# Kernel tuning notes

Hardware: AMD Instinct MI355X
Metric: run time of the kernel (lower is better)

## Reference

```python
import jax, jax.numpy as jnp
import numpy as np

EMBED_DIM = 1024
NUM_HEADS = 16
HEAD_DIM = EMBED_DIM // NUM_HEADS


def setup_inputs() -> dict:
    key = jax.random.key(0)
    ks = jax.random.split(key, 9)
    B, S, E = 4, 2048, EMBED_DIM
    scale = 1.0 / np.sqrt(E)
    x = jax.random.normal(ks[0], (B, S, E), dtype=jnp.float32)
    # Linear layers: weight [E, E] (out, in) and bias [E], torch-style init scale
    Wq = jax.random.uniform(ks[1], (E, E), jnp.float32, -scale, scale)
    bq = jax.random.uniform(ks[2], (E,), jnp.float32, -scale, scale)
    Wk = jax.random.uniform(ks[3], (E, E), jnp.float32, -scale, scale)
    bk = jax.random.uniform(ks[4], (E,), jnp.float32, -scale, scale)
    Wv = jax.random.uniform(ks[5], (E, E), jnp.float32, -scale, scale)
    bv = jax.random.uniform(ks[6], (E,), jnp.float32, -scale, scale)
    Wo = jax.random.uniform(ks[7], (E, E), jnp.float32, -scale, scale)
    bo = jax.random.uniform(ks[8], (E,), jnp.float32, -scale, scale)
    return {"x": x, "Wq": Wq, "bq": bq, "Wk": Wk, "bk": bk,
            "Wv": Wv, "bv": bv, "Wo": Wo, "bo": bo}


def reference(x, Wq, bq, Wk, bk, Wv, bv, Wo, bo):
    B, S, E = x.shape
    H, D = NUM_HEADS, HEAD_DIM

    def proj(W, b):
        # torch Linear: x @ W.T + b ; reshape to [B, H, S, D]
        y = jnp.einsum('bse,fe->bsf', x, W) + b
        return y.reshape(B, S, H, D).transpose(0, 2, 1, 3)

    Q = proj(Wq, bq)
    K = proj(Wk, bk)
    V = proj(Wv, bv)
    scores = jnp.einsum('bhqd,bhkd->bhqk', Q, K) / jnp.sqrt(
        jnp.asarray(D, dtype=jnp.float32))
    attn = jax.nn.softmax(scores, axis=-1)
    out = jnp.einsum('bhqk,bhkd->bhqd', attn, V)
    out = out.transpose(0, 2, 1, 3).reshape(B, S, E)
    out = jnp.einsum('bse,fe->bsf', out, Wo) + bo
    return out
```

## Files before the change

kernel.cpp:

```cpp
#include <hip/hip_runtime.h>
#include <math.h>

#define SEQ 2048
#define EMB 1024
#define NH 16
#define HD 64
#define BATCH 4
#define MROWS (BATCH * SEQ)

typedef unsigned short u16;
typedef unsigned int u32;
typedef _Float16 f16;
using half8   = __attribute__((ext_vector_type(8))) f16;
using fp16x2  = __attribute__((ext_vector_type(2))) __fp16;
using vfloat4 = __attribute__((ext_vector_type(4))) float;

__device__ __forceinline__ u16 f2h(float f) {
    union { f16 h; u16 u; } x; x.h = (f16)f; return x.u;
}
__device__ __forceinline__ u32 pk2h(float a, float b) {
    union { fp16x2 h; u32 u; } x;
    x.h = __builtin_amdgcn_cvt_pkrtz(a, b);
    return x.u;
}
__device__ __forceinline__ float exp2v(float x) {
    float r; asm("v_exp_f32 %0, %1" : "=v"(r) : "v"(x)); return r;
}

__device__ __forceinline__ void gload16(const void* g, void* l) {
    __builtin_amdgcn_global_load_lds(
        (const __attribute__((address_space(1))) void*)g,
        (__attribute__((address_space(3))) void*)l, 16, 0, 0);
}

__global__ __launch_bounds__(256) void cvt5_kernel(
    const float* __restrict__ x,  const float* __restrict__ wq,
    const float* __restrict__ wk, const float* __restrict__ wv,
    const float* __restrict__ wo,
    uint2* __restrict__ xh, uint2* __restrict__ wqkv, uint2* __restrict__ woh)
{
    int gid = blockIdx.x * 256 + threadIdx.x;
    const float4* src; uint2* dst; int o;
    if (gid < (1 << 21)) {
        src = (const float4*)x; dst = xh; o = gid;
    } else {
        int g = gid - (1 << 21);
        int r = g >> 18;
        o = g & ((1 << 18) - 1);
        if      (r == 0) { src = (const float4*)wq; dst = wqkv; }
        else if (r == 1) { src = (const float4*)wk; dst = wqkv + (1 << 18); }
        else if (r == 2) { src = (const float4*)wv; dst = wqkv + (2 << 18); }
        else             { src = (const float4*)wo; dst = woh; }
    }
    float4 v = src[o];
    dst[o] = make_uint2(pk2h(v.x, v.y), pk2h(v.z, v.w));
}

__global__ __launch_bounds__(256) void gemm_qkv_kernel(
    const u16* __restrict__ A, const u16* __restrict__ Wqkv,
    const float* __restrict__ bq, const float* __restrict__ bk,
    const float* __restrict__ bv,
    u16* __restrict__ Qo, u16* __restrict__ Ko, u16* __restrict__ Vo,
    float sq)
{
    __shared__ char lds[32768];
    const int tid = threadIdx.x, wave = tid >> 6, lane = tid & 63;
    const int bm = blockIdx.y, bn = blockIdx.x;
    const int mat = bn >> 3;
    const int wr = wave >> 1, wc = wave & 1;

    const int srow  = wave * 16 + (lane >> 2);
    const int sslot = lane & 3;
    const int ldso  = wave * 1024 + (lane << 4);
    const u16* Ab = A    + (size_t)bm * 128 * EMB;
    const u16* Wb = Wqkv + (size_t)bn * 128 * EMB;

    vfloat4 acc[4][4] = {};

#define QKV_STAGE(k0, bufi)                                                   \
    {                                                                         \
        char* Ad = lds + (bufi) * 16384;                                      \
        char* Bd = Ad + 8192;                                                 \
        _Pragma("unroll")                                                     \
        for (int i2 = 0; i2 < 2; ++i2) {                                      \
            int row = i2 * 64 + srow;                                         \
            int ko  = ((sslot ^ ((row >> 1) & 3)) << 3);                      \
            gload16(Ab + (size_t)row * EMB + (k0) + ko, Ad + i2 * 4096 + ldso); \
            gload16(Wb + (size_t)row * EMB + (k0) + ko, Bd + i2 * 4096 + ldso); \
        }                                                                     \
    }

    QKV_STAGE(0, 0);
    __syncthreads();

    for (int it = 0; it < EMB / 32; ++it) {
        const int cur = it & 1;
        if (it + 1 < EMB / 32) QKV_STAGE((it + 1) * 32, cur ^ 1);

        char* As = lds + cur * 16384;
        char* Bs = As + 8192;
        half8 af[4], bfr[4];
        #pragma unroll
        for (int m = 0; m < 4; ++m) {
            int r = wr * 64 + m * 16 + (lane & 15);
            af[m] = *(const half8*)(As + r * 64 + ((((lane >> 4) ^ ((r >> 1) & 3)) << 4)));
        }
        #pragma unroll
        for (int n = 0; n < 4; ++n) {
            int r = wc * 64 + n * 16 + (lane & 15);
            bfr[n] = *(const half8*)(Bs + r * 64 + ((((lane >> 4) ^ ((r >> 1) & 3)) << 4)));
        }
        #pragma unroll
        for (int m = 0; m < 4; ++m)
            #pragma unroll
            for (int n = 0; n < 4; ++n)
                acc[m][n] = __builtin_amdgcn_mfma_f32_16x16x32_f16(af[m], bfr[n], acc[m][n], 0, 0, 0);

        __syncthreads();
    }
#undef QKV_STAGE

    const float* bp = (mat == 0) ? bq : ((mat == 1) ? bk : bv);
    const float scale = (mat == 0) ? sq : 1.0f;
    u16* Co = (mat == 0) ? Qo : ((mat == 1) ? Ko : Vo);
    const int row0 = bm * 128 + wr * 64;
    const int col0 = (bn & 7) * 128 + wc * 64;

    #pragma unroll
    for (int n = 0; n < 4; ++n) {
        int col = col0 + n * 16 + (lane & 15);
        float bb = bp[col];
        int h = col >> 6, d = col & 63;
        if (mat != 2) {
            #pragma unroll
            for (int m = 0; m < 4; ++m)
                #pragma unroll
                for (int j = 0; j < 4; ++j) {
                    int row = row0 + m * 16 + (lane >> 4) * 4 + j;
                    int b = row >> 11, s = row & (SEQ - 1);
                    Co[(((size_t)(b * NH + h)) * SEQ + s) * HD + d] =
                        f2h((acc[m][n][j] + bb) * scale);
                }
        } else {
            #pragma unroll
            for (int m = 0; m < 4; ++m) {
                int row = row0 + m * 16 + (lane >> 4) * 4;
                int b = row >> 11, s = row & (SEQ - 1);
                u32 w0 = pk2h(acc[m][n][0] + bb, acc[m][n][1] + bb);
                u32 w1 = pk2h(acc[m][n][2] + bb, acc[m][n][3] + bb);
                *(uint2*)(Co + (((size_t)(b * NH + h)) * HD + d) * SEQ + s) =
                    make_uint2(w0, w1);
            }
        }
    }
}

__global__ __launch_bounds__(256) void gemm_f16_kernel(
    const u16* __restrict__ A, const u16* __restrict__ W,
    const float* __restrict__ bias, float* __restrict__ C)
{
    __shared__ char lds[32768];
    const int tid = threadIdx.x, wave = tid >> 6, lane = tid & 63;
    const int bm = blockIdx.y, bn = blockIdx.x;
    const int wr = wave >> 1, wc = wave & 1;

    const int srow  = wave * 16 + (lane >> 2);
    const int sslot = lane & 3;
    const int ldso  = wave * 1024 + (lane << 4);
    const u16* Ab = A + (size_t)bm * 128 * EMB;
    const u16* Wb = W + (size_t)bn * 128 * EMB;

    vfloat4 acc[4][4] = {};

#define F16_STAGE(k0, bufi)                                                   \
    {                                                                         \
        char* Ad = lds + (bufi) * 16384;                                      \
        char* Bd = Ad + 8192;                                                 \
        _Pragma("unroll")                                                     \
        for (int i2 = 0; i2 < 2; ++i2) {                                      \
            int row = i2 * 64 + srow;                                         \
            int ko  = ((sslot ^ ((row >> 1) & 3)) << 3);                      \
            gload16(Ab + (size_t)row * EMB + (k0) + ko, Ad + i2 * 4096 + ldso); \
            gload16(Wb + (size_t)row * EMB + (k0) + ko, Bd + i2 * 4096 + ldso); \
        }                                                                     \
    }

    F16_STAGE(0, 0);
    __syncthreads();

    for (int it = 0; it < EMB / 32; ++it) {
        const int cur = it & 1;
        if (it + 1 < EMB / 32) F16_STAGE((it + 1) * 32, cur ^ 1);

        char* As = lds + cur * 16384;
        char* Bs = As + 8192;
        half8 af[4], bfr[4];
        #pragma unroll
        for (int m = 0; m < 4; ++m) {
            int r = wr * 64 + m * 16 + (lane & 15);
            af[m] = *(const half8*)(As + r * 64 + ((((lane >> 4) ^ ((r >> 1) & 3)) << 4)));
        }
        #pragma unroll
        for (int n = 0; n < 4; ++n) {
            int r = wc * 64 + n * 16 + (lane & 15);
            bfr[n] = *(const half8*)(Bs + r * 64 + ((((lane >> 4) ^ ((r >> 1) & 3)) << 4)));
        }
        #pragma unroll
        for (int m = 0; m < 4; ++m)
            #pragma unroll
            for (int n = 0; n < 4; ++n)
                acc[m][n] = __builtin_amdgcn_mfma_f32_16x16x32_f16(af[m], bfr[n], acc[m][n], 0, 0, 0);

        __syncthreads();
    }
#undef F16_STAGE

    const int row0 = bm * 128 + wr * 64, col0 = bn * 128 + wc * 64;
    #pragma unroll
    for (int n = 0; n < 4; ++n) {
        int col = col0 + n * 16 + (lane & 15);
        float bb = bias[col];
        #pragma unroll
        for (int m = 0; m < 4; ++m)
            #pragma unroll
            for (int j = 0; j < 4; ++j) {
                int row = row0 + m * 16 + (lane >> 4) * 4 + j;
                C[(size_t)row * EMB + col] = acc[m][n][j] + bb;
            }
    }
}

__device__ __forceinline__ void stage_rows(const u16* g, int rstride, char* dst,
                                           int wave, int lane) {
    int r = wave * 8 + (lane >> 3), sl = lane & 7;
    #pragma unroll
    for (int i2 = 0; i2 < 2; ++i2) {
        int row = i2 * 32 + r;
        gload16(g + (size_t)row * rstride + ((sl ^ (row & 7)) << 3),
                dst + i2 * 4096 + wave * 1024 + (lane << 4));
    }
}

__global__ __launch_bounds__(256) void attn_kernel(
    const u16* __restrict__ Q, const u16* __restrict__ K,
    const u16* __restrict__ Vt, u16* __restrict__ O)
{
    __shared__ char lds[40960];
    char* QPs = lds;
    char* Kb0 = lds + 8192;
    char* Kb1 = lds + 16384;
    char* Vb0 = lds + 24576;
    char* Vb1 = lds + 32768;

    const int tid = threadIdx.x, wave = tid >> 6, lane = tid & 63;
    const int c = lane >> 4, li = lane & 15;

    const int swz = (blockIdx.x & 7) * 128 + (blockIdx.x >> 3);
    const int bh = swz >> 4;
    const int q0 = (swz & 15) << 7;

    const u16* Qg = Q  + ((size_t)bh * SEQ + q0) * HD;
    const u16* Kg = K  + (size_t)bh * SEQ * HD;
    const u16* Vg = Vt + (size_t)bh * HD * SEQ;

    stage_rows(Qg, HD, QPs, wave, lane);
    stage_rows(Kg, HD, Kb0, wave, lane);
    stage_rows(Vg, SEQ, Vb0, wave, lane);
    __syncthreads();

    half8 qf[2][2];
    const int q = wave * 16 + li;
    #pragma unroll
    for (int cc = 0; cc < 2; ++cc)
        qf[0][cc] = *(const half8*)(QPs + q * 128 + (((4 * cc + c) ^ (q & 7)) << 4));
    __syncthreads();
    stage_rows(Qg + (size_t)64 * HD, HD, QPs, wave, lane);
    __syncthreads();
    #pragma unroll
    for (int cc = 0; cc < 2; ++cc)
        qf[1][cc] = *(const half8*)(QPs + q * 128 + (((4 * cc + c) ^ (q & 7)) << 4));

    const half8 ones8 = {1, 1, 1, 1, 1, 1, 1, 1};
    char* Pw = QPs + wave * 2048;
    vfloat4 o0[4] = {}, o1[4] = {};
    vfloat4 l0 = {}, l1 = {};

    for (int kt = 0; kt < SEQ / 64; ++kt) {
        char* Kc = (kt & 1) ? Kb1 : Kb0;
        char* Vc = (kt & 1) ? Vb1 : Vb0;
        if (kt < SEQ / 64 - 1) {
            stage_rows(Kg + (size_t)(kt + 1) * 64 * HD, HD,
                       (kt & 1) ? Kb0 : Kb1, wave, lane);
            stage_rows(Vg + (kt + 1) * 64, SEQ,
                       (kt & 1) ? Vb0 : Vb1, wave, lane);
        }

        vfloat4 s0[4] = {}, s1[4] = {};
        __builtin_amdgcn_s_setprio(1);
        #pragma unroll
        for (int n = 0; n < 4; ++n) {
            int key = 16 * n + li;
            #pragma unroll
            for (int cc = 0; cc < 2; ++cc) {
                half8 kb = *(const half8*)(Kc + key * 128 + (((4 * cc + c) ^ (li & 7)) << 4));
                s0[n] = __builtin_amdgcn_mfma_f32_16x16x32_f16(kb, qf[0][cc], s0[n], 0, 0, 0);
                s1[n] = __builtin_amdgcn_mfma_f32_16x16x32_f16(kb, qf[1][cc], s1[n], 0, 0, 0);
            }
        }
        __builtin_amdgcn_s_setprio(0);

        #pragma unroll
        for (int n = 0; n < 4; ++n)
            #pragma unroll
            for (int j = 0; j < 4; ++j) {
                s0[n][j] = exp2v(s0[n][j]);
                s1[n][j] = exp2v(s1[n][j]);
            }

        half8 pf0[2], pf1[2];
        #pragma unroll
        for (int n = 0; n < 4; ++n) {
            u32 w0 = pk2h(s0[n][0], s0[n][1]);
            u32 w1 = pk2h(s0[n][2], s0[n][3]);
            *(uint2*)(Pw + li * 128 + (((2 * n + (c >> 1)) ^ (li & 7)) << 4) + ((c & 1) << 3))
                = make_uint2(w0, w1);
        }
        #pragma unroll
        for (int cc = 0; cc < 2; ++cc)
            pf0[cc] = *(const half8*)(Pw + li * 128 + (((4 * cc + c) ^ (li & 7)) << 4));
        #pragma unroll
        for (int n = 0; n < 4; ++n) {
            u32 w0 = pk2h(s1[n][0], s1[n][1]);
            u32 w1 = pk2h(s1[n][2], s1[n][3]);
            *(uint2*)(Pw + li * 128 + (((2 * n + (c >> 1)) ^ (li & 7)) << 4) + ((c & 1) << 3))
                = make_uint2(w0, w1);
        }
        #pragma unroll
        for (int cc = 0; cc < 2; ++cc)
            pf1[cc] = *(const half8*)(Pw + li * 128 + (((4 * cc + c) ^ (li & 7)) << 4));

        __builtin_amdgcn_s_setprio(1);
        #pragma unroll
        for (int n = 0; n < 4; ++n) {
            int r = 16 * n + li;
            #pragma unroll
            for (int cc = 0; cc < 2; ++cc) {
                half8 vf = *(const half8*)(Vc + r * 128 + (((4 * cc + c) ^ (li & 7)) << 4));
                o0[n] = __builtin_amdgcn_mfma_f32_16x16x32_f16(vf, pf0[cc], o0[n], 0, 0, 0);
                o1[n] = __builtin_amdgcn_mfma_f32_16x16x32_f16(vf, pf1[cc], o1[n], 0, 0, 0);
            }
        }
        #pragma unroll
        for (int cc = 0; cc < 2; ++cc) {
            l0 = __builtin_amdgcn_mfma_f32_16x16x32_f16(ones8, pf0[cc], l0, 0, 0, 0);
            l1 = __builtin_amdgcn_mfma_f32_16x16x32_f16(ones8, pf1[cc], l1, 0, 0, 0);
        }
        __builtin_amdgcn_s_setprio(0);

        __syncthreads();
    }

    const int b = bh >> 4, h = bh & 15;
    const size_t r0 = ((size_t)b * SEQ + q0 + wave * 16 + li) * EMB + h * 64;
    const size_t r1 = ((size_t)b * SEQ + q0 + 64 + wave * 16 + li) * EMB + h * 64;
    float i0 = 1.0f / l0[0];
    float i1 = 1.0f / l1[0];
    #pragma unroll
    for (int n = 0; n < 4; ++n) {
        *(uint2*)(O + r0 + 16 * n + 4 * c) =
            make_uint2(pk2h(o0[n][0] * i0, o0[n][1] * i0),
                       pk2h(o0[n][2] * i0, o0[n][3] * i0));
        *(uint2*)(O + r1 + 16 * n + 4 * c) =
            make_uint2(pk2h(o1[n][0] * i1, o1[n][1] * i1),
                       pk2h(o1[n][2] * i1, o1[n][3] * i1));
    }
}

extern "C" void kernel_launch(void* const* d_in, const int* in_sizes, int n_in,
                              void* d_out, int out_size, void* d_ws, size_t ws_size,
                              hipStream_t stream) {
    const float* x  = (const float*)d_in[0];
    const float* Wq = (const float*)d_in[1];
    const float* bq = (const float*)d_in[2];
    const float* Wk = (const float*)d_in[3];
    const float* bk = (const float*)d_in[4];
    const float* Wv = (const float*)d_in[5];
    const float* bv = (const float*)d_in[6];
    const float* Wo = (const float*)d_in[7];
    const float* bo = (const float*)d_in[8];
    float* out = (float*)d_out;

    char* ws = (char*)d_ws;
    u16* xh   = (u16*)(ws);
    u16* Qh   = (u16*)(ws + ((size_t)16 << 20));
    u16* Kh   = (u16*)(ws + ((size_t)32 << 20));
    u16* Vh   = (u16*)(ws + ((size_t)48 << 20));
    u16* Ah   = (u16*)(ws + ((size_t)64 << 20));
    u16* Wqkv = (u16*)(ws + ((size_t)80 << 20));
    u16* Woh  = (u16*)(ws + ((size_t)88 << 20));

    const int nCvt = (1 << 21) + (1 << 20);

    cvt5_kernel<<<nCvt / 256, 256, 0, stream>>>(
        x, Wq, Wk, Wv, Wo, (uint2*)xh, (uint2*)Wqkv, (uint2*)Woh);

    const float SCALE_Q = 0.125f * 1.4426950408889634f;
    gemm_qkv_kernel<<<dim3(3 * EMB / 128, MROWS / 128), 256, 0, stream>>>(
        xh, Wqkv, bq, bk, bv, Qh, Kh, Vh, SCALE_Q);

    attn_kernel<<<dim3(SEQ / 128 * BATCH * NH), 256, 0, stream>>>(Qh, Kh, Vh, Ah);

    gemm_f16_kernel<<<dim3(EMB / 128, MROWS / 128), 256, 0, stream>>>(Ah, Woh, bo, out);
}
```

Measured before the change: 214.6 us.

## Split P scratch into two buffers and use partial vmcnt waits with raw barriers

Gives each of the two query halves its own LDS region for the P tile, so both writes can be issued before both reads instead of a serialised write-read-write-read on one buffer. The full __syncthreads at the end of each key tile is replaced by raw s_barrier instructions plus an explicit s_waitcnt vmcnt(4) at the top of the loop. This lets the prefetch of the next K/V tile stay in flight while the current tile is consumed. It raises LDS use from 40 KB to 48 KB, which may lower occupancy, and correctness depends on the hand-counted vmcnt matching the number of outstanding global-to-LDS loads.

New measurement: 219.9 us. 2.5% more time.

```diff
diff --git a/kernel.cpp b/kernel.cpp
--- a/kernel.cpp
+++ b/kernel.cpp
@@ -245,12 +245,13 @@
     const u16* __restrict__ Q, const u16* __restrict__ K,
     const u16* __restrict__ Vt, u16* __restrict__ O)
 {
-    __shared__ char lds[40960];
-    char* QPs = lds;
-    char* Kb0 = lds + 8192;
-    char* Kb1 = lds + 16384;
-    char* Vb0 = lds + 24576;
-    char* Vb1 = lds + 32768;
+    __shared__ char lds[49152];
+    char* Ps0 = lds;
+    char* Ps1 = lds + 8192;
+    char* Kb0 = lds + 16384;
+    char* Kb1 = lds + 24576;
+    char* Vb0 = lds + 32768;
+    char* Vb1 = lds + 40960;
 
     const int tid = threadIdx.x, wave = tid >> 6, lane = tid & 63;
     const int c = lane >> 4, li = lane & 15;
@@ -263,7 +264,7 @@
     const u16* Kg = K  + (size_t)bh * SEQ * HD;
     const u16* Vg = Vt + (size_t)bh * HD * SEQ;
 
-    stage_rows(Qg, HD, QPs, wave, lane);
+    stage_rows(Qg, HD, Ps0, wave, lane);
     stage_rows(Kg, HD, Kb0, wave, lane);
     stage_rows(Vg, SEQ, Vb0, wave, lane);
     __syncthreads();
@@ -272,16 +273,17 @@
     const int q = wave * 16 + li;
     #pragma unroll
     for (int cc = 0; cc < 2; ++cc)
-        qf[0][cc] = *(const half8*)(QPs + q * 128 + (((4 * cc + c) ^ (q & 7)) << 4));
+        qf[0][cc] = *(const half8*)(Ps0 + q * 128 + (((4 * cc + c) ^ (q & 7)) << 4));
     __syncthreads();
-    stage_rows(Qg + (size_t)64 * HD, HD, QPs, wave, lane);
+    stage_rows(Qg + (size_t)64 * HD, HD, Ps0, wave, lane);
     __syncthreads();
     #pragma unroll
     for (int cc = 0; cc < 2; ++cc)
-        qf[1][cc] = *(const half8*)(QPs + q * 128 + (((4 * cc + c) ^ (q & 7)) << 4));
+        qf[1][cc] = *(const half8*)(Ps0 + q * 128 + (((4 * cc + c) ^ (q & 7)) << 4));
 
     const half8 ones8 = {1, 1, 1, 1, 1, 1, 1, 1};
-    char* Pw = QPs + wave * 2048;
+    char* Pw0 = Ps0 + wave * 2048;
+    char* Pw1 = Ps1 + wave * 2048;
     vfloat4 o0[4] = {}, o1[4] = {};
     vfloat4 l0 = {}, l1 = {};
 
@@ -293,7 +295,12 @@
                        (kt & 1) ? Kb0 : Kb1, wave, lane);
             stage_rows(Vg + (kt + 1) * 64, SEQ,
                        (kt & 1) ? Vb0 : Vb1, wave, lane);
-        }
+            asm volatile("s_waitcnt vmcnt(4)" ::: "memory");
+        } else {
+            asm volatile("s_waitcnt vmcnt(0)" ::: "memory");
+        }
+        __builtin_amdgcn_sched_barrier(0);
+        asm volatile("s_barrier" ::: "memory");
 
         vfloat4 s0[4] = {}, s1[4] = {};
         __builtin_amdgcn_s_setprio(1);
@@ -317,27 +324,19 @@
                 s1[n][j] = exp2v(s1[n][j]);
             }
 
+        #pragma unroll
+        for (int n = 0; n < 4; ++n) {
+            *(uint2*)(Pw0 + li * 128 + (((2 * n + (c >> 1)) ^ (li & 7)) << 4) + ((c & 1) << 3))
+                = make_uint2(pk2h(s0[n][0], s0[n][1]), pk2h(s0[n][2], s0[n][3]));
+            *(uint2*)(Pw1 + li * 128 + (((2 * n + (c >> 1)) ^ (li & 7)) << 4) + ((c & 1) << 3))
+                = make_uint2(pk2h(s1[n][0], s1[n][1]), pk2h(s1[n][2], s1[n][3]));
+        }
         half8 pf0[2], pf1[2];
         #pragma unroll
-        for (int n = 0; n < 4; ++n) {
-            u32 w0 = pk2h(s0[n][0], s0[n][1]);
-            u32 w1 = pk2h(s0[n][2], s0[n][3]);
-            *(uint2*)(Pw + li * 128 + (((2 * n + (c >> 1)) ^ (li & 7)) << 4) + ((c & 1) << 3))
-                = make_uint2(w0, w1);
-        }
-        #pragma unroll
-        for (int cc = 0; cc < 2; ++cc)
-            pf0[cc] = *(const half8*)(Pw + li * 128 + (((4 * cc + c) ^ (li & 7)) << 4));
-        #pragma unroll
-        for (int n = 0; n < 4; ++n) {
-            u32 w0 = pk2h(s1[n][0], s1[n][1]);
-            u32 w1 = pk2h(s1[n][2], s1[n][3]);
-            *(uint2*)(Pw + li * 128 + (((2 * n + (c >> 1)) ^ (li & 7)) << 4) + ((c & 1) << 3))
-                = make_uint2(w0, w1);
-        }
-        #pragma unroll
-        for (int cc = 0; cc < 2; ++cc)
-            pf1[cc] = *(const half8*)(Pw + li * 128 + (((4 * cc + c) ^ (li & 7)) << 4));
+        for (int cc = 0; cc < 2; ++cc) {
+            pf0[cc] = *(const half8*)(Pw0 + li * 128 + (((4 * cc + c) ^ (li & 7)) << 4));
+            pf1[cc] = *(const half8*)(Pw1 + li * 128 + (((4 * cc + c) ^ (li & 7)) << 4));
+        }
 
         __builtin_amdgcn_s_setprio(1);
         #pragma unroll
@@ -357,7 +356,7 @@
         }
         __builtin_amdgcn_s_setprio(0);
 
-        __syncthreads();
+        asm volatile("s_barrier" ::: "memory");
     }
 
     const int b = bh >> 4, h = bh & 15;
```
